# Optimization experiments

Measured on AMD Instinct MI355X. Metric: run time of the kernel, lower is better.

## Reference

```python
import jax, jax.numpy as jnp
import numpy as np

LN_EPS = 1e-5
DEN_EPS = 1e-5


def _layernorm(x, gamma, beta):
    mu = jnp.mean(x, axis=-1, keepdims=True)
    var = jnp.mean((x - mu) ** 2, axis=-1, keepdims=True)
    return (x - mu) * jax.lax.rsqrt(var + LN_EPS) * gamma + beta


def setup_inputs() -> dict:
    key = jax.random.key(0)
    ks = jax.random.split(key, 10)
    B, T, Fin, D = 4, 1024, 256, 128
    s = 0.02
    return {
        "x": jax.random.normal(ks[0], (B, T, Fin), jnp.float32),
        "S0": jnp.zeros((B, 1, D, D), jnp.float32),
        "Z0": jnp.zeros((B, 1, D), jnp.float32),
        "ln_gamma": jnp.ones((Fin,), jnp.float32),
        "ln_beta": jnp.zeros((Fin,), jnp.float32),
        "Wk": jax.random.normal(ks[1], (D, Fin), jnp.float32) * s,
        "Wq": jax.random.normal(ks[2], (D, Fin), jnp.float32) * s,
        "Wv": jax.random.normal(ks[3], (D, Fin), jnp.float32) * s,
        "W1": jax.random.normal(ks[4], (D, D), jnp.float32) * s,
        "b1": jnp.zeros((D,), jnp.float32),
        "W2": jax.random.normal(ks[5], (D, D), jnp.float32) * s,
        "b2": jnp.zeros((D,), jnp.float32),
        "Ws": jax.random.normal(ks[6], (D, Fin), jnp.float32) * s,
        "bs": jnp.zeros((D,), jnp.float32),
    }


def reference(x, S0, Z0, ln_gamma, ln_beta, Wk, Wq, Wv, W1, b1, W2, b2, Ws, bs):
    xn = _layernorm(x, ln_gamma, ln_beta)            # [B,T,Fin]
    phi = lambda z: jax.nn.elu(z) + 1.0
    K = phi(jnp.einsum('btf,df->btd', xn, Wk))       # [B,T,D]
    Q = phi(jnp.einsum('btf,df->btd', xn, Wq))
    V = jnp.einsum('btf,df->btd', xn, Wv)
    # running-sum aggregation of K outer V, seeded by carried state
    KV = jnp.einsum('bti,btj->btij', K, V)           # [B,T,D,D]
    S = jnp.cumsum(KV, axis=1) + S0                  # [B,T,D,D]
    Z = jnp.cumsum(K, axis=1) + Z0                   # [B,T,D]
    num = jnp.einsum('bti,btil->btl', Q, S)          # [B,T,D]
    den = jnp.einsum('btl,btl->bt', Q, Z)[..., None] + DEN_EPS
    out = num / den
    out = jax.nn.relu(jnp.einsum('btd,ed->bte', out, W1) + b1)
    out = jax.nn.relu(jnp.einsum('btd,ed->bte', out, W2) + b2)
    out = out + jnp.einsum('btf,df->btd', xn, Ws) + bs
    return (out, S, Z)
```

## Files before the change

kernel.cpp:

```cpp
#include <hip/hip_runtime.h>
#include <math.h>

#define BB 4
#define TT 1024
#define FIN 256
#define DD 128
#define CL 16
#define NC 64
#define ROWS (BB*TT)

__global__ __launch_bounds__(256) void k_ln_qkv(
    const float* __restrict__ x, const float* __restrict__ gamma, const float* __restrict__ beta,
    const float* __restrict__ Wk, const float* __restrict__ Wq, const float* __restrict__ Wv,
    const float* __restrict__ Ws, const float* __restrict__ bs,
    float* __restrict__ Kp, float* __restrict__ Qp, float* __restrict__ Vp, float* __restrict__ XSp)
{
    __shared__ float xt[8][FIN];
    const int tid  = threadIdx.x;
    const int row0 = blockIdx.x * 8;

    {
        const int r = tid >> 5, l = tid & 31;
        const float* xr = x + (size_t)(row0 + r) * FIN + l * 8;
        float v[8];
        #pragma unroll
        for (int k = 0; k < 8; ++k) v[k] = xr[k];
        float s = 0.f, sq = 0.f;
        #pragma unroll
        for (int k = 0; k < 8; ++k) { s += v[k]; sq += v[k] * v[k]; }
        #pragma unroll
        for (int m = 16; m >= 1; m >>= 1) {
            s  += __shfl_xor(s,  m, 64);
            sq += __shfl_xor(sq, m, 64);
        }
        const float mu  = s * (1.0f / FIN);
        const float var = sq * (1.0f / FIN) - mu * mu;
        const float rs  = rsqrtf(var + 1e-5f);
        #pragma unroll
        for (int k = 0; k < 8; ++k) {
            const int f = l * 8 + k;
            xt[r][f] = (v[k] - mu) * rs * gamma[f] + beta[f];
        }
    }
    __syncthreads();

    const int m0 = tid >> 7;
    const int d  = tid & 127;
    const int m1 = (tid + 256) >> 7;
    const float* W0 = (m0 == 0 ? Wk : Wq) + (size_t)d * FIN;
    const float* W1r = (m1 == 2 ? Wv : Ws) + (size_t)d * FIN;

    float acc0[8], acc1[8];
    #pragma unroll
    for (int r = 0; r < 8; ++r) { acc0[r] = 0.f; acc1[r] = 0.f; }

    for (int k4 = 0; k4 < FIN / 4; ++k4) {
        const float4 w0 = ((const float4*)W0)[k4];
        const float4 w1 = ((const float4*)W1r)[k4];
        #pragma unroll
        for (int r = 0; r < 8; ++r) {
            const float4 xv = ((const float4*)xt[r])[k4];
            acc0[r] += w0.x * xv.x + w0.y * xv.y + w0.z * xv.z + w0.w * xv.w;
            acc1[r] += w1.x * xv.x + w1.y * xv.y + w1.z * xv.z + w1.w * xv.w;
        }
    }

    float* dst0 = (m0 == 0 ? Kp : Qp);
    float* dst1 = (m1 == 2 ? Vp : XSp);
    const float bsv = (m1 == 3) ? bs[d] : 0.f;
    #pragma unroll
    for (int r = 0; r < 8; ++r) {
        float a = acc0[r];
        a = (a > 0.f) ? (a + 1.f) : expf(a);
        dst0[(size_t)(row0 + r) * DD + d] = a;
        dst1[(size_t)(row0 + r) * DD + d] = acc1[r] + bsv;
    }
}

__global__ __launch_bounds__(256) void k_chunksum(
    const float* __restrict__ Kp, const float* __restrict__ Vp,
    float* __restrict__ SKV, float* __restrict__ SK)
{
    __shared__ float Kb[CL][DD];
    __shared__ float Vb[CL][DD];
    const int tid = threadIdx.x;
    const int c = blockIdx.x & (NC - 1);
    const int b = blockIdx.x >> 6;
    const size_t base = (size_t)(b * TT + c * CL) * DD;

    #pragma unroll
    for (int q = 0; q < 2; ++q) {
        const int fi = q * 256 + tid;
        ((float4*)&Kb[0][0])[fi] = ((const float4*)(Kp + base))[fi];
        ((float4*)&Vb[0][0])[fi] = ((const float4*)(Vp + base))[fi];
    }
    __syncthreads();

    const int j = tid & 127, hi = tid >> 7;
    float acc[64];
    #pragma unroll
    for (int w = 0; w < 64; ++w) acc[w] = 0.f;

    for (int t = 0; t < CL; ++t) {
        const float vj = Vb[t][j];
        #pragma unroll
        for (int w4 = 0; w4 < 16; ++w4) {
            const float4 kf = *(const float4*)&Kb[t][hi * 64 + w4 * 4];
            acc[w4 * 4 + 0] += kf.x * vj;
            acc[w4 * 4 + 1] += kf.y * vj;
            acc[w4 * 4 + 2] += kf.z * vj;
            acc[w4 * 4 + 3] += kf.w * vj;
        }
    }

    float* out = SKV + (size_t)(b * NC + c) * DD * DD;
    #pragma unroll
    for (int w = 0; w < 64; ++w) {
        const int i = hi * 64 + w;
        out[(size_t)i * DD + j] = acc[w];
    }
    if (tid < DD) {
        float s = 0.f;
        #pragma unroll
        for (int t = 0; t < CL; ++t) s += Kb[t][tid];
        SK[(size_t)(b * NC + c) * DD + tid] = s;
    }
}

__global__ __launch_bounds__(256) void k_prefix(
    const float* __restrict__ SKV, const float* __restrict__ SK,
    const float* __restrict__ S0, const float* __restrict__ Z0,
    float* __restrict__ Sout, float* __restrict__ Zout)
{
    const int gid = blockIdx.x * 256 + threadIdx.x;
    const int b = gid >> 14, e = gid & 16383;
    float acc = S0[(size_t)b * 16384 + e];
    const float* p = SKV + (size_t)b * NC * 16384 + e;
    float* so = Sout + (size_t)b * TT * 16384 + (size_t)(CL - 1) * 16384 + e;
    for (int c = 0; c < NC; ++c) {
        acc += p[(size_t)c * 16384];
        so[(size_t)c * CL * 16384] = acc;
    }
    if (gid < BB * DD) {
        const int b2 = gid >> 7, i = gid & 127;
        float z = Z0[b2 * DD + i];
        for (int c = 0; c < NC; ++c) {
            z += SK[(size_t)(b2 * NC + c) * DD + i];
            Zout[(size_t)(b2 * TT + c * CL + CL - 1) * DD + i] = z;
        }
    }
}

__global__ __launch_bounds__(256) void k_scan(
    const float* __restrict__ Kp, const float* __restrict__ Qp, const float* __restrict__ Vp,
    const float* __restrict__ S0, const float* __restrict__ Z0,
    float* __restrict__ Sout, float* __restrict__ Zout, float* __restrict__ NUM)
{
    __shared__ float Kb[CL][DD];
    __shared__ float Qb[CL][DD];
    __shared__ float Vb[CL][64];
    __shared__ float4 nred[2][4][16];

    const int tid  = threadIdx.x;
    const int half = blockIdx.x & 1;
    const int c    = (blockIdx.x >> 1) & (NC - 1);
    const int b    = blockIdx.x >> 7;
    const int j0   = half * 64;
    const size_t rbase = (size_t)(b * TT + c * CL);

    {
        const float4* Ksrc = (const float4*)(Kp + rbase * DD);
        const float4* Qsrc = (const float4*)(Qp + rbase * DD);
        #pragma unroll
        for (int q = 0; q < 2; ++q) {
            const int fi = q * 256 + tid;
            ((float4*)&Kb[0][0])[fi] = Ksrc[fi];
            ((float4*)&Qb[0][0])[fi] = Qsrc[fi];
        }
        const int tv = tid >> 4, gv = tid & 15;
        ((float4*)&Vb[0][0])[tid] = *(const float4*)(Vp + (rbase + tv) * DD + j0 + gv * 4);
    }

    const int g = tid & 15, h = tid >> 4;
    float4 acc[8];
    {
        const float* src = (c == 0) ? (S0 + (size_t)b * 16384)
                                    : (Sout + ((size_t)(b * TT) + c * CL - 1) * 16384);
        #pragma unroll
        for (int w = 0; w < 8; ++w) {
            const int i = w * 16 + h;
            acc[w] = *(const float4*)(src + (size_t)i * DD + j0 + g * 4);
        }
    }
    float zacc = 0.f;
    const bool doZ = (half == 0) && (tid < DD);
    if (doZ) {
        zacc = (c == 0) ? Z0[b * DD + tid]
                        : Zout[((size_t)(b * TT) + c * CL - 1) * DD + tid];
    }
    __syncthreads();

    const int wav = tid >> 6;
    for (int t = 0; t < CL; ++t) {
        const size_t tt = rbase + t;
        const float4 v4 = *(const float4*)&Vb[t][g * 4];
        float4 np; np.x = np.y = np.z = np.w = 0.f;
        float* srow = Sout + tt * 16384 + j0 + g * 4;
        #pragma unroll
        for (int w = 0; w < 8; ++w) {
            const int i = w * 16 + h;
            const float kk = Kb[t][i];
            const float qq = Qb[t][i];
            acc[w].x += kk * v4.x; acc[w].y += kk * v4.y;
            acc[w].z += kk * v4.z; acc[w].w += kk * v4.w;
            if (t < CL - 1) *(float4*)(srow + (size_t)i * DD) = acc[w];
            np.x += qq * acc[w].x; np.y += qq * acc[w].y;
            np.z += qq * acc[w].z; np.w += qq * acc[w].w;
        }
        #pragma unroll
        for (int m = 16; m <= 32; m <<= 1) {
            np.x += __shfl_xor(np.x, m, 64);
            np.y += __shfl_xor(np.y, m, 64);
            np.z += __shfl_xor(np.z, m, 64);
            np.w += __shfl_xor(np.w, m, 64);
        }
        if ((tid & 63) < 16) nred[t & 1][wav][g] = np;
        if (doZ) {
            zacc += Kb[t][tid];
            if (t < CL - 1) Zout[tt * DD + tid] = zacc;
        }
        __syncthreads();
        if (tid < 16) {
            const float4 r0 = nred[t & 1][0][tid], r1 = nred[t & 1][1][tid];
            const float4 r2 = nred[t & 1][2][tid], r3 = nred[t & 1][3][tid];
            float4 o;
            o.x = r0.x + r1.x + r2.x + r3.x;
            o.y = r0.y + r1.y + r2.y + r3.y;
            o.z = r0.z + r1.z + r2.z + r3.z;
            o.w = r0.w + r1.w + r2.w + r3.w;
            *(float4*)(NUM + tt * DD + j0 + tid * 4) = o;
        }
    }
}

__global__ __launch_bounds__(256) void k_mlp(
    const float* __restrict__ NUM, const float* __restrict__ Qp,
    const float* __restrict__ Zp, const float* __restrict__ XSp,
    const float* __restrict__ W1, const float* __restrict__ b1,
    const float* __restrict__ W2, const float* __restrict__ b2,
    float* __restrict__ Oout)
{
    __shared__ float h0[16][DD];
    __shared__ float h1[16][DD];
    __shared__ float parr[16][256];
    __shared__ float denl[16];
    const int tid = threadIdx.x;
    const int d = tid & 127, s = tid >> 7;
    const int row0 = blockIdx.x * 16;

    float4 w1r[16], w2r[16];
    #pragma unroll
    for (int k4 = 0; k4 < 16; ++k4) {
        w1r[k4] = *(const float4*)(W1 + (size_t)d * DD + s * 64 + k4 * 4);
        w2r[k4] = *(const float4*)(W2 + (size_t)d * DD + s * 64 + k4 * 4);
    }

    {
        const int r = tid >> 4, kk = tid & 15;
        const float* qrow = Qp + (size_t)(row0 + r) * DD + kk * 8;
        const float* zrow = Zp + (size_t)(row0 + r) * DD + kk * 8;
        float sden = 0.f;
        #pragma unroll
        for (int u = 0; u < 8; ++u) sden += qrow[u] * zrow[u];
        #pragma unroll
        for (int m = 1; m <= 8; m <<= 1) sden += __shfl_xor(sden, m, 64);
        if (kk == 0) denl[r] = sden + 1e-5f;
    }
    __syncthreads();

    #pragma unroll
    for (int q = 0; q < 8; ++q) {
        const int f = q * 256 + tid;
        const int r = f >> 7, dd2 = f & 127;
        h0[r][dd2] = NUM[(size_t)row0 * DD + f] / denl[r];
    }
    __syncthreads();

    #pragma unroll
    for (int r = 0; r < 16; ++r) {
        float pp = 0.f;
        #pragma unroll
        for (int k4 = 0; k4 < 16; ++k4) {
            const float4 xv = *(const float4*)&h0[r][s * 64 + k4 * 4];
            pp += w1r[k4].x * xv.x + w1r[k4].y * xv.y + w1r[k4].z * xv.z + w1r[k4].w * xv.w;
        }
        parr[r][tid] = pp;
    }
    __syncthreads();
    #pragma unroll
    for (int q = 0; q < 8; ++q) {
        const int f = q * 256 + tid;
        const int r = f >> 7, dd2 = f & 127;
        h1[r][dd2] = fmaxf(parr[r][dd2] + parr[r][dd2 + 128] + b1[dd2], 0.f);
    }
    __syncthreads();

    #pragma unroll
    for (int r = 0; r < 16; ++r) {
        float pp = 0.f;
        #pragma unroll
        for (int k4 = 0; k4 < 16; ++k4) {
            const float4 xv = *(const float4*)&h1[r][s * 64 + k4 * 4];
            pp += w2r[k4].x * xv.x + w2r[k4].y * xv.y + w2r[k4].z * xv.z + w2r[k4].w * xv.w;
        }
        parr[r][tid] = pp;
    }
    __syncthreads();
    #pragma unroll
    for (int q = 0; q < 8; ++q) {
        const int f = q * 256 + tid;
        const int r = f >> 7, dd2 = f & 127;
        const float hv = fmaxf(parr[r][dd2] + parr[r][dd2 + 128] + b2[dd2], 0.f);
        Oout[(size_t)row0 * DD + f] = hv + XSp[(size_t)row0 * DD + f];
    }
}

extern "C" void kernel_launch(void* const* d_in, const int* in_sizes, int n_in,
                              void* d_out, int out_size, void* d_ws, size_t ws_size,
                              hipStream_t stream)
{
    const float* x  = (const float*)d_in[0];
    const float* S0 = (const float*)d_in[1];
    const float* Z0 = (const float*)d_in[2];
    const float* g  = (const float*)d_in[3];
    const float* be = (const float*)d_in[4];
    const float* Wk = (const float*)d_in[5];
    const float* Wq = (const float*)d_in[6];
    const float* Wv = (const float*)d_in[7];
    const float* W1 = (const float*)d_in[8];
    const float* b1 = (const float*)d_in[9];
    const float* W2 = (const float*)d_in[10];
    const float* b2 = (const float*)d_in[11];
    const float* Ws = (const float*)d_in[12];
    const float* bs = (const float*)d_in[13];

    float* outp = (float*)d_out;
    float* Sout = outp + (size_t)ROWS * DD;
    float* Zout = Sout + (size_t)BB * TT * DD * DD;

    float* ws  = (float*)d_ws;
    float* Kp  = ws;
    float* Qp  = Kp + (size_t)ROWS * DD;
    float* Vp  = Qp + (size_t)ROWS * DD;
    float* XSp = Vp + (size_t)ROWS * DD;
    float* NUM = XSp + (size_t)ROWS * DD;
    float* SKV = NUM + (size_t)ROWS * DD;
    float* SK  = SKV + (size_t)BB * NC * DD * DD;

    k_ln_qkv  <<<ROWS / 8, 256, 0, stream>>>(x, g, be, Wk, Wq, Wv, Ws, bs, Kp, Qp, Vp, XSp);
    k_chunksum<<<BB * NC, 256, 0, stream>>>(Kp, Vp, SKV, SK);
    k_prefix  <<<BB * DD * DD / 256, 256, 0, stream>>>(SKV, SK, S0, Z0, Sout, Zout);
    k_scan    <<<BB * NC * 2, 256, 0, stream>>>(Kp, Qp, Vp, S0, Z0, Sout, Zout, NUM);
    k_mlp     <<<ROWS / 16, 256, 0, stream>>>(NUM, Qp, Zout, XSp, W1, b1, W2, b2, outp);
}
```

Before: 380.5 us.

## Compute numerator via chunked attention form and fuse with MLP, split S writes

The scan kernel no longer computes the per-step Q·S numerator. A new fused kernel computes num and den per chunk as Q·S_prev plus a causal intra-chunk QK^T·V term, then applies the MLP directly, which removes the NUM workspace round trip and a per-timestep block barrier. The prefix kernel is unrolled by four with loads prefetched ahead to expose more memory parallelism. In exchange, the fused kernel launches only 256 blocks, and each one reads the 64KB chunk-start state from global memory with limited parallelism.

```diff
diff --git a/kernel.cpp b/kernel.cpp
--- a/kernel.cpp
+++ b/kernel.cpp
@@ -8,6 +8,7 @@
 #define CL 16
 #define NC 64
 #define ROWS (BB*TT)
+#define DDP (DD+4)
 
 __global__ __launch_bounds__(256) void k_ln_qkv(
     const float* __restrict__ x, const float* __restrict__ gamma, const float* __restrict__ beta,
@@ -47,7 +48,7 @@
     const int m0 = tid >> 7;
     const int d  = tid & 127;
     const int m1 = (tid + 256) >> 7;
-    const float* W0 = (m0 == 0 ? Wk : Wq) + (size_t)d * FIN;
+    const float* W0  = (m0 == 0 ? Wk : Wq) + (size_t)d * FIN;
     const float* W1r = (m1 == 2 ? Wv : Ws) + (size_t)d * FIN;
 
     float acc0[8], acc1[8];
@@ -136,11 +137,25 @@
     const int b = gid >> 14, e = gid & 16383;
     float acc = S0[(size_t)b * 16384 + e];
     const float* p = SKV + (size_t)b * NC * 16384 + e;
-    float* so = Sout + (size_t)b * TT * 16384 + (size_t)(CL - 1) * 16384 + e;
-    for (int c = 0; c < NC; ++c) {
-        acc += p[(size_t)c * 16384];
-        so[(size_t)c * CL * 16384] = acc;
-    }
+    float* so = Sout + ((size_t)b * TT + CL - 1) * 16384 + e;
+
+    float v0 = p[0], v1 = p[16384], v2 = p[2 * 16384], v3 = p[3 * 16384];
+    for (int c4 = 0; c4 < 16; ++c4) {
+        float n0 = 0.f, n1 = 0.f, n2 = 0.f, n3 = 0.f;
+        if (c4 < 15) {
+            const float* pn = p + (size_t)(c4 * 4 + 4) * 16384;
+            n0 = pn[0]; n1 = pn[16384]; n2 = pn[2 * 16384]; n3 = pn[3 * 16384];
+        }
+        const float a0 = acc + v0, a1 = a0 + v1, a2 = a1 + v2, a3 = a2 + v3;
+        float* s4 = so + (size_t)(c4 * 4) * CL * 16384;
+        s4[0] = a0;
+        s4[(size_t)CL * 16384]     = a1;
+        s4[(size_t)2 * CL * 16384] = a2;
+        s4[(size_t)3 * CL * 16384] = a3;
+        acc = a3;
+        v0 = n0; v1 = n1; v2 = n2; v3 = n3;
+    }
+
     if (gid < BB * DD) {
         const int b2 = gid >> 7, i = gid & 127;
         float z = Z0[b2 * DD + i];
@@ -151,15 +166,13 @@
     }
 }
 
-__global__ __launch_bounds__(256) void k_scan(
-    const float* __restrict__ Kp, const float* __restrict__ Qp, const float* __restrict__ Vp,
+__global__ __launch_bounds__(256) void k_swrite(
+    const float* __restrict__ Kp, const float* __restrict__ Vp,
     const float* __restrict__ S0, const float* __restrict__ Z0,
-    float* __restrict__ Sout, float* __restrict__ Zout, float* __restrict__ NUM)
+    float* Sout, float* Zout)
 {
     __shared__ float Kb[CL][DD];
-    __shared__ float Qb[CL][DD];
     __shared__ float Vb[CL][64];
-    __shared__ float4 nred[2][4][16];
 
     const int tid  = threadIdx.x;
     const int half = blockIdx.x & 1;
@@ -170,22 +183,20 @@
 
     {
         const float4* Ksrc = (const float4*)(Kp + rbase * DD);
-        const float4* Qsrc = (const float4*)(Qp + rbase * DD);
         #pragma unroll
         for (int q = 0; q < 2; ++q) {
             const int fi = q * 256 + tid;
             ((float4*)&Kb[0][0])[fi] = Ksrc[fi];
-            ((float4*)&Qb[0][0])[fi] = Qsrc[fi];
         }
         const int tv = tid >> 4, gv = tid & 15;
-        ((float4*)&Vb[0][0])[tid] = *(const float4*)(Vp + (rbase + tv) * DD + j0 + gv * 4);
+        *(float4*)&Vb[tv][gv * 4] = *(const float4*)(Vp + (rbase + tv) * DD + j0 + gv * 4);
     }
 
     const int g = tid & 15, h = tid >> 4;
     float4 acc[8];
     {
         const float* src = (c == 0) ? (S0 + (size_t)b * 16384)
-                                    : (Sout + ((size_t)(b * TT) + c * CL - 1) * 16384);
+                                    : (Sout + (rbase - 1) * 16384);
         #pragma unroll
         for (int w = 0; w < 8; ++w) {
             const int i = w * 16 + h;
@@ -196,105 +207,137 @@
     const bool doZ = (half == 0) && (tid < DD);
     if (doZ) {
         zacc = (c == 0) ? Z0[b * DD + tid]
-                        : Zout[((size_t)(b * TT) + c * CL - 1) * DD + tid];
-    }
-    __syncthreads();
-
-    const int wav = tid >> 6;
-    for (int t = 0; t < CL; ++t) {
-        const size_t tt = rbase + t;
+                        : Zout[(rbase - 1) * DD + tid];
+    }
+    __syncthreads();
+
+    #pragma unroll
+    for (int t = 0; t < CL - 1; ++t) {
         const float4 v4 = *(const float4*)&Vb[t][g * 4];
-        float4 np; np.x = np.y = np.z = np.w = 0.f;
-        float* srow = Sout + tt * 16384 + j0 + g * 4;
+        float* srow = Sout + (rbase + t) * 16384 + j0 + g * 4;
         #pragma unroll
         for (int w = 0; w < 8; ++w) {
             const int i = w * 16 + h;
             const float kk = Kb[t][i];
-            const float qq = Qb[t][i];
             acc[w].x += kk * v4.x; acc[w].y += kk * v4.y;
             acc[w].z += kk * v4.z; acc[w].w += kk * v4.w;
-            if (t < CL - 1) *(float4*)(srow + (size_t)i * DD) = acc[w];
-            np.x += qq * acc[w].x; np.y += qq * acc[w].y;
-            np.z += qq * acc[w].z; np.w += qq * acc[w].w;
-        }
-        #pragma unroll
-        for (int m = 16; m <= 32; m <<= 1) {
-            np.x += __shfl_xor(np.x, m, 64);
-            np.y += __shfl_xor(np.y, m, 64);
-            np.z += __shfl_xor(np.z, m, 64);
-            np.w += __shfl_xor(np.w, m, 64);
-        }
-        if ((tid & 63) < 16) nred[t & 1][wav][g] = np;
+            *(float4*)(srow + (size_t)i * DD) = acc[w];
+        }
         if (doZ) {
             zacc += Kb[t][tid];
-            if (t < CL - 1) Zout[tt * DD + tid] = zacc;
-        }
-        __syncthreads();
-        if (tid < 16) {
-            const float4 r0 = nred[t & 1][0][tid], r1 = nred[t & 1][1][tid];
-            const float4 r2 = nred[t & 1][2][tid], r3 = nred[t & 1][3][tid];
-            float4 o;
-            o.x = r0.x + r1.x + r2.x + r3.x;
-            o.y = r0.y + r1.y + r2.y + r3.y;
-            o.z = r0.z + r1.z + r2.z + r3.z;
-            o.w = r0.w + r1.w + r2.w + r3.w;
-            *(float4*)(NUM + tt * DD + j0 + tid * 4) = o;
-        }
-    }
-}
-
-__global__ __launch_bounds__(256) void k_mlp(
-    const float* __restrict__ NUM, const float* __restrict__ Qp,
-    const float* __restrict__ Zp, const float* __restrict__ XSp,
+            Zout[(rbase + t) * DD + tid] = zacc;
+        }
+    }
+}
+
+__global__ __launch_bounds__(256) void k_numden_mlp(
+    const float* __restrict__ Kp, const float* __restrict__ Qp, const float* __restrict__ Vp,
+    const float* __restrict__ XSp, const float* __restrict__ S0, const float* __restrict__ Z0,
+    const float* __restrict__ Sout, const float* __restrict__ Zout,
     const float* __restrict__ W1, const float* __restrict__ b1,
     const float* __restrict__ W2, const float* __restrict__ b2,
     float* __restrict__ Oout)
 {
-    __shared__ float h0[16][DD];
-    __shared__ float h1[16][DD];
-    __shared__ float parr[16][256];
-    __shared__ float denl[16];
+    __shared__ float Qs[CL][DDP];
+    __shared__ float Ks[CL][DDP];
+    __shared__ float Vs[CL][DD];
+    __shared__ float As[CL][CL];
+    __shared__ float Zs[DD];
+    __shared__ float den[CL];
+    __shared__ float h0[CL][DD];
+    __shared__ float h1[CL][DD];
+    __shared__ float parr[CL][256];
+
     const int tid = threadIdx.x;
-    const int d = tid & 127, s = tid >> 7;
-    const int row0 = blockIdx.x * 16;
-
-    float4 w1r[16], w2r[16];
-    #pragma unroll
-    for (int k4 = 0; k4 < 16; ++k4) {
-        w1r[k4] = *(const float4*)(W1 + (size_t)d * DD + s * 64 + k4 * 4);
-        w2r[k4] = *(const float4*)(W2 + (size_t)d * DD + s * 64 + k4 * 4);
-    }
-
-    {
-        const int r = tid >> 4, kk = tid & 15;
-        const float* qrow = Qp + (size_t)(row0 + r) * DD + kk * 8;
-        const float* zrow = Zp + (size_t)(row0 + r) * DD + kk * 8;
-        float sden = 0.f;
-        #pragma unroll
-        for (int u = 0; u < 8; ++u) sden += qrow[u] * zrow[u];
-        #pragma unroll
-        for (int m = 1; m <= 8; m <<= 1) sden += __shfl_xor(sden, m, 64);
-        if (kk == 0) denl[r] = sden + 1e-5f;
-    }
-    __syncthreads();
-
-    #pragma unroll
-    for (int q = 0; q < 8; ++q) {
-        const int f = q * 256 + tid;
-        const int r = f >> 7, dd2 = f & 127;
-        h0[r][dd2] = NUM[(size_t)row0 * DD + f] / denl[r];
-    }
-    __syncthreads();
-
-    #pragma unroll
-    for (int r = 0; r < 16; ++r) {
-        float pp = 0.f;
-        #pragma unroll
-        for (int k4 = 0; k4 < 16; ++k4) {
-            const float4 xv = *(const float4*)&h0[r][s * 64 + k4 * 4];
-            pp += w1r[k4].x * xv.x + w1r[k4].y * xv.y + w1r[k4].z * xv.z + w1r[k4].w * xv.w;
-        }
-        parr[r][tid] = pp;
+    const int c = blockIdx.x & (NC - 1);
+    const int b = blockIdx.x >> 6;
+    const size_t rbase = (size_t)(b * TT + c * CL);
+
+    {
+        const float4* Qsrc = (const float4*)(Qp + rbase * DD);
+        const float4* Ksrc = (const float4*)(Kp + rbase * DD);
+        const float4* Vsrc = (const float4*)(Vp + rbase * DD);
+        #pragma unroll
+        for (int q = 0; q < 2; ++q) {
+            const int fi = q * 256 + tid;
+            const int row = fi >> 5, c4 = fi & 31;
+            *(float4*)&Qs[row][c4 * 4] = Qsrc[fi];
+            *(float4*)&Ks[row][c4 * 4] = Ksrc[fi];
+            ((float4*)&Vs[0][0])[fi]   = Vsrc[fi];
+        }
+        if (tid < DD)
+            Zs[tid] = (c == 0) ? Z0[b * DD + tid] : Zout[(rbase - 1) * DD + tid];
+    }
+    __syncthreads();
+
+    {
+        const int r = tid >> 4, t2 = tid & 15;
+        float s = 0.f;
+        #pragma unroll
+        for (int k4 = 0; k4 < DD / 4; ++k4) {
+            const float4 q4 = *(const float4*)&Qs[r][k4 * 4];
+            const float4 k4v = *(const float4*)&Ks[t2][k4 * 4];
+            s += q4.x * k4v.x + q4.y * k4v.y + q4.z * k4v.z + q4.w * k4v.w;
+        }
+        As[r][t2] = s;
+    }
+    __syncthreads();
+    if (tid < CL) {
+        const int r = tid;
+        float s = 1e-5f;
+        #pragma unroll
+        for (int k = 0; k < DD; ++k) s += Qs[r][k] * Zs[k];
+        #pragma unroll
+        for (int t2 = 0; t2 < CL; ++t2) if (t2 <= r) s += As[r][t2];
+        den[r] = s;
+    }
+    __syncthreads();
+
+    {
+        const int r = tid >> 4;
+        const int jq = (tid & 15) * 8;
+        float4 a0 = {0, 0, 0, 0}, a1 = {0, 0, 0, 0};
+        const float* Sstart = (c == 0) ? (S0 + (size_t)b * 16384)
+                                       : (Sout + (rbase - 1) * 16384);
+        for (int i = 0; i < DD; ++i) {
+            const float qv = Qs[r][i];
+            const float4 s0v = *(const float4*)(Sstart + (size_t)i * DD + jq);
+            const float4 s1v = *(const float4*)(Sstart + (size_t)i * DD + jq + 4);
+            a0.x += qv * s0v.x; a0.y += qv * s0v.y; a0.z += qv * s0v.z; a0.w += qv * s0v.w;
+            a1.x += qv * s1v.x; a1.y += qv * s1v.y; a1.z += qv * s1v.z; a1.w += qv * s1v.w;
+        }
+        #pragma unroll
+        for (int t2 = 0; t2 < CL; ++t2) {
+            const float av = (t2 <= r) ? As[r][t2] : 0.f;
+            const float4 v0 = *(const float4*)&Vs[t2][jq];
+            const float4 v1 = *(const float4*)&Vs[t2][jq + 4];
+            a0.x += av * v0.x; a0.y += av * v0.y; a0.z += av * v0.z; a0.w += av * v0.w;
+            a1.x += av * v1.x; a1.y += av * v1.y; a1.z += av * v1.z; a1.w += av * v1.w;
+        }
+        const float rd = 1.0f / den[r];
+        a0.x *= rd; a0.y *= rd; a0.z *= rd; a0.w *= rd;
+        a1.x *= rd; a1.y *= rd; a1.z *= rd; a1.w *= rd;
+        *(float4*)&h0[r][jq]     = a0;
+        *(float4*)&h0[r][jq + 4] = a1;
+    }
+    __syncthreads();
+
+    const int d = tid & 127, sh = tid >> 7;
+    {
+        float4 w1r[16];
+        #pragma unroll
+        for (int k4 = 0; k4 < 16; ++k4)
+            w1r[k4] = *(const float4*)(W1 + (size_t)d * DD + sh * 64 + k4 * 4);
+        #pragma unroll
+        for (int r = 0; r < CL; ++r) {
+            float pp = 0.f;
+            #pragma unroll
+            for (int k4 = 0; k4 < 16; ++k4) {
+                const float4 xv = *(const float4*)&h0[r][sh * 64 + k4 * 4];
+                pp += w1r[k4].x * xv.x + w1r[k4].y * xv.y + w1r[k4].z * xv.z + w1r[k4].w * xv.w;
+            }
+            parr[r][tid] = pp;
+        }
     }
     __syncthreads();
     #pragma unroll
@@ -304,16 +347,21 @@
         h1[r][dd2] = fmaxf(parr[r][dd2] + parr[r][dd2 + 128] + b1[dd2], 0.f);
     }
     __syncthreads();
-
-    #pragma unroll
-    for (int r = 0; r < 16; ++r) {
-        float pp = 0.f;
-        #pragma unroll
-        for (int k4 = 0; k4 < 16; ++k4) {
-            const float4 xv = *(const float4*)&h1[r][s * 64 + k4 * 4];
-            pp += w2r[k4].x * xv.x + w2r[k4].y * xv.y + w2r[k4].z * xv.z + w2r[k4].w * xv.w;
-        }
-        parr[r][tid] = pp;
+    {
+        float4 w2r[16];
+        #pragma unroll
+        for (int k4 = 0; k4 < 16; ++k4)
+            w2r[k4] = *(const float4*)(W2 + (size_t)d * DD + sh * 64 + k4 * 4);
+        #pragma unroll
+        for (int r = 0; r < CL; ++r) {
+            float pp = 0.f;
+            #pragma unroll
+            for (int k4 = 0; k4 < 16; ++k4) {
+                const float4 xv = *(const float4*)&h1[r][sh * 64 + k4 * 4];
+                pp += w2r[k4].x * xv.x + w2r[k4].y * xv.y + w2r[k4].z * xv.z + w2r[k4].w * xv.w;
+            }
+            parr[r][tid] = pp;
+        }
     }
     __syncthreads();
     #pragma unroll
@@ -321,7 +369,7 @@
         const int f = q * 256 + tid;
         const int r = f >> 7, dd2 = f & 127;
         const float hv = fmaxf(parr[r][dd2] + parr[r][dd2 + 128] + b2[dd2], 0.f);
-        Oout[(size_t)row0 * DD + f] = hv + XSp[(size_t)row0 * DD + f];
+        Oout[rbase * DD + f] = hv + XSp[rbase * DD + f];
     }
 }
 
@@ -353,13 +401,13 @@
     float* Qp  = Kp + (size_t)ROWS * DD;
     float* Vp  = Qp + (size_t)ROWS * DD;
     float* XSp = Vp + (size_t)ROWS * DD;
-    float* NUM = XSp + (size_t)ROWS * DD;
-    float* SKV = NUM + (size_t)ROWS * DD;
+    float* SKV = XSp + (size_t)ROWS * DD;
     float* SK  = SKV + (size_t)BB * NC * DD * DD;
 
-    k_ln_qkv  <<<ROWS / 8, 256, 0, stream>>>(x, g, be, Wk, Wq, Wv, Ws, bs, Kp, Qp, Vp, XSp);
-    k_chunksum<<<BB * NC, 256, 0, stream>>>(Kp, Vp, SKV, SK);
-    k_prefix  <<<BB * DD * DD / 256, 256, 0, stream>>>(SKV, SK, S0, Z0, Sout, Zout);
-    k_scan    <<<BB * NC * 2, 256, 0, stream>>>(Kp, Qp, Vp, S0, Z0, Sout, Zout, NUM);
-    k_mlp     <<<ROWS / 16, 256, 0, stream>>>(NUM, Qp, Zout, XSp, W1, b1, W2, b2, outp);
-}
+    k_ln_qkv    <<<ROWS / 8, 256, 0, stream>>>(x, g, be, Wk, Wq, Wv, Ws, bs, Kp, Qp, Vp, XSp);
+    k_chunksum  <<<BB * NC, 256, 0, stream>>>(Kp, Vp, SKV, SK);
+    k_prefix    <<<BB * DD * DD / 256, 256, 0, stream>>>(SKV, SK, S0, Z0, Sout, Zout);
+    k_swrite    <<<BB * NC * 2, 256, 0, stream>>>(Kp, Vp, S0, Z0, Sout, Zout);
+    k_numden_mlp<<<BB * NC, 256, 0, stream>>>(Kp, Qp, Vp, XSp, S0, Z0, Sout, Zout,
+                                              W1, b1, W2, b2, outp);
+}
```

Measured after the change: 396.4 us. +4.2%, slower.
